# Kernel tuning notes

Measured on AMD Instinct MI355X. Metric: run time of the kernel, lower is better.

Reference implementation:

```python
import jax, jax.numpy as jnp
import numpy as np

N = 50000   # nodes
E = 800000  # edges (avg degree 16)
D = 64      # feature dim (in == out, so lin_self is Identity)
NEG_SLOPE = 0.2


def setup_inputs() -> dict:
    key = jax.random.key(0)
    ks = jax.random.split(key, 8)
    s = 1.0 / np.sqrt(D)
    return {
        "x": jax.random.normal(ks[0], (N, D), dtype=jnp.float32),
        "edge_index": jax.random.randint(ks[1], (2, E), 0, N, dtype=jnp.int64),
        "edge_attr": jax.random.uniform(ks[2], (E,), dtype=jnp.float32),
        "W_msg": jax.random.normal(ks[3], (D, D), dtype=jnp.float32) * s,
        "b_msg": jax.random.normal(ks[4], (D,), dtype=jnp.float32) * s,
        "W_edge": jax.random.normal(ks[5], (1, D), dtype=jnp.float32),
        "b_edge": jax.random.normal(ks[6], (D,), dtype=jnp.float32),
        "att": jax.random.normal(ks[7], (D,), dtype=jnp.float32) * s,
    }


def reference(x, edge_index, edge_attr, W_msg, b_msg, W_edge, b_edge, att):
    src, dst = edge_index[0], edge_index[1]
    # message: lin_msg(x_j) + lin_edge(edge_attr)           [E, D]
    msg = x[src] @ W_msg + b_msg + edge_attr[:, None] @ W_edge + b_edge
    # additive attention logits (heads=1)                   [E]
    logits = jnp.sum(jax.nn.leaky_relu(msg, NEG_SLOPE) * att, axis=-1)
    # segment softmax over destination nodes (PyG softmax, eps=1e-16)
    m = jax.ops.segment_max(logits, dst, num_segments=N)
    m = jnp.where(jnp.isneginf(m), 0.0, m)
    ex = jnp.exp(logits - m[dst])
    denom = jax.ops.segment_sum(ex, dst, num_segments=N)
    alpha = ex / (denom[dst] + 1e-16)
    weighted = msg * alpha[:, None]
    # scatter-max aggregation; empty segments -> 0 (PyG fill value)
    agg = jax.ops.segment_max(weighted, dst, num_segments=N)
    agg = jnp.where(jnp.isneginf(agg), 0.0, agg)
    # lin_self is Identity (in_channels == out_channels, skip_linear=False)
    return agg + x
```

## Files before the change

### kernel.cpp

```cpp
#include <hip/hip_runtime.h>

#define N_NODES 50000
#define N_EDGES 800000
#define DIM 64
#define NEG_SLOPE 0.2f
#define NEG_INF (-__builtin_inff())
#define NB      3125
#define MAXDEG  128

typedef _Float16 half8 __attribute__((ext_vector_type(8)));

__global__ __launch_bounds__(256) void k_pre(const float* __restrict__ x,
                                             const float* __restrict__ W,
                                             const float* __restrict__ b_msg,
                                             const float* __restrict__ b_edge,
                                             _Float16* __restrict__ xmh,
                                             const int* __restrict__ eidx,
                                             const float* __restrict__ eattr,
                                             unsigned* __restrict__ cnt,
                                             int2* __restrict__ elist) {
    __shared__ float Ws[DIM * DIM];
    __shared__ float xs[16 * DIM];
    int tid = threadIdx.x;
    int bid = blockIdx.x;

    int e = bid * 256 + tid;
    int    esrc = eidx[e];
    int    edst = eidx[N_EDGES + e];
    float  ea   = eattr[e];
    unsigned r  = atomicAdd(cnt + edst, 1u);

    const float4* W4 = (const float4*)W;
    float4* Ws4 = (float4*)Ws;
    #pragma unroll
    for (int i = 0; i < 4; ++i) Ws4[tid + 256 * i] = W4[tid + 256 * i];
    int base = bid * 16;
    ((float4*)xs)[tid] = ((const float4*)(x + (size_t)base * DIM))[tid];
    __syncthreads();

    if (r < MAXDEG)
        elist[((size_t)edst << 7) + r] = make_int2(esrc, __float_as_int(ea));

    int w = tid >> 6;
    int d = tid & 63;
    float bias = b_msg[d] + b_edge[d];
    float s0 = bias, s1 = bias, s2 = bias, s3 = bias;
    const float* xr = xs + (w * 4) * DIM;
    #pragma unroll
    for (int k = 0; k < DIM; ++k) {
        float wv = Ws[k * DIM + d];
        s0 = fmaf(xr[k], wv, s0);
        s1 = fmaf(xr[DIM + k], wv, s1);
        s2 = fmaf(xr[2 * DIM + k], wv, s2);
        s3 = fmaf(xr[3 * DIM + k], wv, s3);
    }
    _Float16* o = xmh + ((size_t)base + w * 4) * DIM + d;
    o[0] = (_Float16)s0;
    o[DIM] = (_Float16)s1;
    o[2 * DIM] = (_Float16)s2;
    o[3 * DIM] = (_Float16)s3;
}

__global__ __launch_bounds__(256) void k_aggregate(const half8* __restrict__ xm8,
                                                   const int2* __restrict__ elist,
                                                   const unsigned* __restrict__ cnt,
                                                   const float4* __restrict__ W_edge4,
                                                   const float4* __restrict__ att4,
                                                   const float4* __restrict__ x4,
                                                   float4* __restrict__ out4) {
    int lane = threadIdx.x & 63;
    int wv   = threadIdx.x >> 6;
    int g = lane >> 3, t = lane & 7;
    int node = (blockIdx.x * 4 + wv) * 8 + g;
    if (node >= N_NODES) return;
    unsigned deg = cnt[node];
    if (deg > MAXDEG) deg = MAXDEG;
    size_t obase = (size_t)node * 16 + 2 * t;
    if (deg == 0) {
        out4[obase] = x4[obase];
        out4[obase + 1] = x4[obase + 1];
        return;
    }
    float4 wa = W_edge4[2 * t], wb = W_edge4[2 * t + 1];
    float4 aa = att4[2 * t],    ab = att4[2 * t + 1];
    float we[8] = {wa.x, wa.y, wa.z, wa.w, wb.x, wb.y, wb.z, wb.w};
    float at[8] = {aa.x, aa.y, aa.z, aa.w, ab.x, ab.y, ab.z, ab.w};

    unsigned beg = (unsigned)node << 7;
    int2  e = elist[beg];
    half8 h = xm8[(size_t)e.x * 8 + t];

    float m = NEG_INF, denom = 0.f;
    float v[8];
    #pragma unroll
    for (int k = 0; k < 8; ++k) v[k] = 0.f;

    unsigned i = 0;
    while (true) {
        bool more = (i + 1) < deg;
        int2 e2; half8 h2;
        if (more) {
            e2 = elist[beg + i + 1];
            h2 = xm8[(size_t)e2.x * 8 + t];
        }
        float ea = __int_as_float(e.y);
        float msg[8];
        float p = 0.f;
        #pragma unroll
        for (int k = 0; k < 8; ++k) {
            float f = (float)h[k];
            msg[k] = fmaf(ea, we[k], f);
            float lr = fmaxf(msg[k], NEG_SLOPE * msg[k]);
            p = fmaf(lr, at[k], p);
        }
        p += __shfl_xor(p, 1, 64);
        p += __shfl_xor(p, 2, 64);
        p += __shfl_xor(p, 4, 64);
        if (i == 0) {
            m = p; denom = 1.f;
            #pragma unroll
            for (int k = 0; k < 8; ++k) v[k] = msg[k];
        } else {
            float M  = fmaxf(m, p);
            float so = __expf(m - M);
            float sn = __expf(p - M);
            denom = fmaf(denom, so, sn);
            #pragma unroll
            for (int k = 0; k < 8; ++k)
                v[k] = fmaxf(v[k] * so, msg[k] * sn);
            m = M;
        }
        if (!more) break;
        e = e2; h = h2; ++i;
    }
    float inv = 1.0f / (denom + 1e-16f);
    float4 xa = x4[obase], xb = x4[obase + 1];
    float4 r0, r1;
    r0.x = fmaf(v[0], inv, xa.x);
    r0.y = fmaf(v[1], inv, xa.y);
    r0.z = fmaf(v[2], inv, xa.z);
    r0.w = fmaf(v[3], inv, xa.w);
    r1.x = fmaf(v[4], inv, xb.x);
    r1.y = fmaf(v[5], inv, xb.y);
    r1.z = fmaf(v[6], inv, xb.z);
    r1.w = fmaf(v[7], inv, xb.w);
    out4[obase] = r0;
    out4[obase + 1] = r1;
}

extern "C" void kernel_launch(void* const* d_in, const int* in_sizes, int n_in,
                              void* d_out, int out_size, void* d_ws, size_t ws_size,
                              hipStream_t stream) {
    const float* x      = (const float*)d_in[0];
    const int*   eidx   = (const int*)d_in[1];
    const float* eattr  = (const float*)d_in[2];
    const float* W_msg  = (const float*)d_in[3];
    const float* b_msg  = (const float*)d_in[4];
    const float* W_edge = (const float*)d_in[5];
    const float* b_edge = (const float*)d_in[6];
    const float* att    = (const float*)d_in[7];
    float* out = (float*)d_out;

    _Float16* xmh   = (_Float16*)d_ws;
    int2*     elist = (int2*)(xmh + (size_t)N_NODES * DIM);
    unsigned* cnt   = (unsigned*)(elist + (size_t)N_NODES * MAXDEG);

    hipMemsetAsync(cnt, 0, (size_t)N_NODES * 4, stream);

    k_pre<<<NB, 256, 0, stream>>>(x, W_msg, b_msg, b_edge, xmh,
                                  eidx, eattr, cnt, elist);
    k_aggregate<<<(N_NODES + 31) / 32, 256, 0, stream>>>(
        (const half8*)xmh, elist, cnt, (const float4*)W_edge,
        (const float4*)att, (const float4*)x, (float4*)out);
}
```

Baseline: 154.4 us.

## Bin edges by 64-node destination groups into segmented buckets, regroup in LDS

Edges are no longer scattered to a per-node padded list. They are appended to per-bin (64 destination nodes), per-segment buckets, which cuts atomic contention and makes the scattered writes more local. The aggregate kernel now runs one block per bin: it loads that bin's records into shared memory, builds per-node index lists with LDS atomics, and then runs the same online softmax/max loop. The cost is an extra shared-memory regroup step and capacity limits (256 records per segment) that could drop edges for skewed inputs. Edge order within a node also becomes nondeterministic.

```diff
diff --git a/kernel.cpp b/kernel.cpp
--- a/kernel.cpp
+++ b/kernel.cpp
@@ -6,6 +6,9 @@
 #define NEG_SLOPE 0.2f
 #define NEG_INF (-__builtin_inff())
 #define NB      3125
+#define NBIN    782
+#define SEGS    8
+#define SEGCAP  256
 #define MAXDEG  128
 
 typedef _Float16 half8 __attribute__((ext_vector_type(8)));
@@ -17,18 +20,20 @@
                                              _Float16* __restrict__ xmh,
                                              const int* __restrict__ eidx,
                                              const float* __restrict__ eattr,
-                                             unsigned* __restrict__ cnt,
-                                             int2* __restrict__ elist) {
+                                             unsigned* __restrict__ tails,
+                                             int2* __restrict__ rec) {
     __shared__ float Ws[DIM * DIM];
     __shared__ float xs[16 * DIM];
     int tid = threadIdx.x;
     int bid = blockIdx.x;
 
     int e = bid * 256 + tid;
+    int    edst = eidx[N_EDGES + e];
     int    esrc = eidx[e];
-    int    edst = eidx[N_EDGES + e];
     float  ea   = eattr[e];
-    unsigned r  = atomicAdd(cnt + edst, 1u);
+    int bin = edst >> 6;
+    int seg = bid & 7;
+    unsigned slot = atomicAdd(tails + (bin * SEGS + seg), 1u);
 
     const float4* W4 = (const float4*)W;
     float4* Ws4 = (float4*)Ws;
@@ -38,8 +43,9 @@
     ((float4*)xs)[tid] = ((const float4*)(x + (size_t)base * DIM))[tid];
     __syncthreads();
 
-    if (r < MAXDEG)
-        elist[((size_t)edst << 7) + r] = make_int2(esrc, __float_as_int(ea));
+    if (slot < SEGCAP)
+        rec[(size_t)(bin * SEGS + seg) * SEGCAP + slot] =
+            make_int2((esrc << 6) | (edst & 63), __float_as_int(ea));
 
     int w = tid >> 6;
     int d = tid & 63;
@@ -62,90 +68,125 @@
 }
 
 __global__ __launch_bounds__(256) void k_aggregate(const half8* __restrict__ xm8,
-                                                   const int2* __restrict__ elist,
-                                                   const unsigned* __restrict__ cnt,
+                                                   const int2* __restrict__ rec,
+                                                   const unsigned* __restrict__ tails,
                                                    const float4* __restrict__ W_edge4,
                                                    const float4* __restrict__ att4,
                                                    const float4* __restrict__ x4,
                                                    float4* __restrict__ out4) {
-    int lane = threadIdx.x & 63;
-    int wv   = threadIdx.x >> 6;
+    __shared__ int2 rs[SEGS * SEGCAP];
+    __shared__ unsigned short lst[64 * MAXDEG];
+    __shared__ unsigned degs[64];
+    __shared__ unsigned scnt[SEGS];
+    int tid = threadIdx.x;
+    int bin = blockIdx.x;
+
+    if (tid < SEGS) {
+        unsigned c = tails[bin * SEGS + tid];
+        scnt[tid] = c > SEGCAP ? SEGCAP : c;
+    }
+    if (tid < 64) degs[tid] = 0;
+    __syncthreads();
+
+    #pragma unroll
+    for (int s = 0; s < SEGS * SEGCAP; s += 256) {
+        int slot = s + tid;
+        int seg = slot >> 8, i = slot & 255;
+        if ((unsigned)i < scnt[seg]) {
+            int2 r = rec[(size_t)(bin * SEGS + seg) * SEGCAP + i];
+            rs[slot] = r;
+            unsigned nr = (unsigned)r.x & 63u;
+            unsigned k = atomicAdd(&degs[nr], 1u);
+            if (k < MAXDEG) lst[nr * MAXDEG + k] = (unsigned short)slot;
+        }
+    }
+    __syncthreads();
+
+    int lane = tid & 63;
+    int wvi  = tid >> 6;
     int g = lane >> 3, t = lane & 7;
-    int node = (blockIdx.x * 4 + wv) * 8 + g;
-    if (node >= N_NODES) return;
-    unsigned deg = cnt[node];
-    if (deg > MAXDEG) deg = MAXDEG;
-    size_t obase = (size_t)node * 16 + 2 * t;
-    if (deg == 0) {
-        out4[obase] = x4[obase];
-        out4[obase + 1] = x4[obase + 1];
-        return;
-    }
+    int gid = wvi * 8 + g;
+
     float4 wa = W_edge4[2 * t], wb = W_edge4[2 * t + 1];
     float4 aa = att4[2 * t],    ab = att4[2 * t + 1];
     float we[8] = {wa.x, wa.y, wa.z, wa.w, wb.x, wb.y, wb.z, wb.w};
     float at[8] = {aa.x, aa.y, aa.z, aa.w, ab.x, ab.y, ab.z, ab.w};
 
-    unsigned beg = (unsigned)node << 7;
-    int2  e = elist[beg];
-    half8 h = xm8[(size_t)e.x * 8 + t];
-
-    float m = NEG_INF, denom = 0.f;
-    float v[8];
-    #pragma unroll
-    for (int k = 0; k < 8; ++k) v[k] = 0.f;
-
-    unsigned i = 0;
-    while (true) {
-        bool more = (i + 1) < deg;
-        int2 e2; half8 h2;
-        if (more) {
-            e2 = elist[beg + i + 1];
-            h2 = xm8[(size_t)e2.x * 8 + t];
+    #pragma unroll
+    for (int half = 0; half < 2; ++half) {
+        int rr = gid + half * 32;
+        int node = bin * 64 + rr;
+        if (node >= N_NODES) continue;
+        unsigned deg = degs[rr];
+        if (deg > MAXDEG) deg = MAXDEG;
+        size_t obase = (size_t)node * 16 + 2 * t;
+        if (deg == 0) {
+            out4[obase] = x4[obase];
+            out4[obase + 1] = x4[obase + 1];
+            continue;
         }
-        float ea = __int_as_float(e.y);
-        float msg[8];
-        float p = 0.f;
+        const unsigned short* L = lst + rr * MAXDEG;
+        int2 r = rs[L[0]];
+        float ea = __int_as_float(r.y);
+        half8 h  = xm8[(size_t)((unsigned)r.x >> 6) * 8 + t];
+
+        float m = NEG_INF, denom = 0.f;
+        float v[8];
         #pragma unroll
-        for (int k = 0; k < 8; ++k) {
-            float f = (float)h[k];
-            msg[k] = fmaf(ea, we[k], f);
-            float lr = fmaxf(msg[k], NEG_SLOPE * msg[k]);
-            p = fmaf(lr, at[k], p);
+        for (int k = 0; k < 8; ++k) v[k] = 0.f;
+
+        unsigned i = 0;
+        while (true) {
+            bool more = (i + 1) < deg;
+            float ea2; half8 h2;
+            if (more) {
+                int2 r2 = rs[L[i + 1]];
+                ea2 = __int_as_float(r2.y);
+                h2  = xm8[(size_t)((unsigned)r2.x >> 6) * 8 + t];
+            }
+            float msg[8];
+            float p = 0.f;
+            #pragma unroll
+            for (int k = 0; k < 8; ++k) {
+                float f = (float)h[k];
+                msg[k] = fmaf(ea, we[k], f);
+                float lr = fmaxf(msg[k], NEG_SLOPE * msg[k]);
+                p = fmaf(lr, at[k], p);
+            }
+            p += __shfl_xor(p, 1, 64);
+            p += __shfl_xor(p, 2, 64);
+            p += __shfl_xor(p, 4, 64);
+            if (i == 0) {
+                m = p; denom = 1.f;
+                #pragma unroll
+                for (int k = 0; k < 8; ++k) v[k] = msg[k];
+            } else {
+                float M  = fmaxf(m, p);
+                float so = __expf(m - M);
+                float sn = __expf(p - M);
+                denom = fmaf(denom, so, sn);
+                #pragma unroll
+                for (int k = 0; k < 8; ++k)
+                    v[k] = fmaxf(v[k] * so, msg[k] * sn);
+                m = M;
+            }
+            if (!more) break;
+            ea = ea2; h = h2; ++i;
         }
-        p += __shfl_xor(p, 1, 64);
-        p += __shfl_xor(p, 2, 64);
-        p += __shfl_xor(p, 4, 64);
-        if (i == 0) {
-            m = p; denom = 1.f;
-            #pragma unroll
-            for (int k = 0; k < 8; ++k) v[k] = msg[k];
-        } else {
-            float M  = fmaxf(m, p);
-            float so = __expf(m - M);
-            float sn = __expf(p - M);
-            denom = fmaf(denom, so, sn);
-            #pragma unroll
-            for (int k = 0; k < 8; ++k)
-                v[k] = fmaxf(v[k] * so, msg[k] * sn);
-            m = M;
-        }
-        if (!more) break;
-        e = e2; h = h2; ++i;
-    }
-    float inv = 1.0f / (denom + 1e-16f);
-    float4 xa = x4[obase], xb = x4[obase + 1];
-    float4 r0, r1;
-    r0.x = fmaf(v[0], inv, xa.x);
-    r0.y = fmaf(v[1], inv, xa.y);
-    r0.z = fmaf(v[2], inv, xa.z);
-    r0.w = fmaf(v[3], inv, xa.w);
-    r1.x = fmaf(v[4], inv, xb.x);
-    r1.y = fmaf(v[5], inv, xb.y);
-    r1.z = fmaf(v[6], inv, xb.z);
-    r1.w = fmaf(v[7], inv, xb.w);
-    out4[obase] = r0;
-    out4[obase + 1] = r1;
+        float inv = 1.0f / (denom + 1e-16f);
+        float4 xa = x4[obase], xb = x4[obase + 1];
+        float4 r0, r1;
+        r0.x = fmaf(v[0], inv, xa.x);
+        r0.y = fmaf(v[1], inv, xa.y);
+        r0.z = fmaf(v[2], inv, xa.z);
+        r0.w = fmaf(v[3], inv, xa.w);
+        r1.x = fmaf(v[4], inv, xb.x);
+        r1.y = fmaf(v[5], inv, xb.y);
+        r1.z = fmaf(v[6], inv, xb.z);
+        r1.w = fmaf(v[7], inv, xb.w);
+        out4[obase] = r0;
+        out4[obase + 1] = r1;
+    }
 }
 
 extern "C" void kernel_launch(void* const* d_in, const int* in_sizes, int n_in,
@@ -162,14 +203,14 @@
     float* out = (float*)d_out;
 
     _Float16* xmh   = (_Float16*)d_ws;
-    int2*     elist = (int2*)(xmh + (size_t)N_NODES * DIM);
-    unsigned* cnt   = (unsigned*)(elist + (size_t)N_NODES * MAXDEG);
-
-    hipMemsetAsync(cnt, 0, (size_t)N_NODES * 4, stream);
+    int2*     rec   = (int2*)(xmh + (size_t)N_NODES * DIM);
+    unsigned* tails = (unsigned*)(rec + (size_t)NBIN * SEGS * SEGCAP);
+
+    hipMemsetAsync(tails, 0, (size_t)NBIN * SEGS * 4, stream);
 
     k_pre<<<NB, 256, 0, stream>>>(x, W_msg, b_msg, b_edge, xmh,
-                                  eidx, eattr, cnt, elist);
-    k_aggregate<<<(N_NODES + 31) / 32, 256, 0, stream>>>(
-        (const half8*)xmh, elist, cnt, (const float4*)W_edge,
+                                  eidx, eattr, tails, rec);
+    k_aggregate<<<NBIN, 256, 0, stream>>>(
+        (const half8*)xmh, rec, tails, (const float4*)W_edge,
         (const float4*)att, (const float4*)x, (float4*)out);
 }
```

Result: slower. 157.9 us (+2.2%).
